# Performance work log

Measured on AMD Instinct MI355X. Metric: run time of the kernel, lower is better.

The kernel has to match this reference:

```python
import jax, jax.numpy as jnp
from jax import lax
import numpy as np

B, TIN, F, H, TOUT = 256, 512, 64, 512, 64


def setup_inputs() -> dict:
    key = jax.random.key(0)
    ks = jax.random.split(key, 16)
    s = 0.05

    def p(k, shape):
        return jax.random.normal(k, shape, jnp.float32) * s

    inp = {
        "x": jax.random.normal(ks[0], (B, TIN, F), jnp.float32),
        "y": jax.random.normal(ks[1], (B, TOUT), jnp.float32),
    }
    i = 2
    for name, insz in [("enc0", F), ("enc1", H), ("dec0", 1), ("dec1", H)]:
        inp[name + "_Wih"] = p(ks[i], (4 * H, insz)); i += 1
        inp[name + "_Whh"] = p(ks[i], (4 * H, H)); i += 1
        inp[name + "_bih"] = jnp.zeros((4 * H,), jnp.float32)
        inp[name + "_bhh"] = jnp.zeros((4 * H,), jnp.float32)
    inp["proj_W"] = p(ks[i], (1, H)); i += 1
    inp["proj_b"] = jnp.zeros((1,), jnp.float32)
    return inp


def _cell(xt, h, c, Wih, Whh, bih, bhh):
    # PyTorch gate order: i, f, g, o
    g = xt @ Wih.T + h @ Whh.T + bih + bhh  # [B, 4H]
    i, f, gg, o = jnp.split(g, 4, axis=-1)
    c = jax.nn.sigmoid(f) * c + jax.nn.sigmoid(i) * jnp.tanh(gg)
    h = jax.nn.sigmoid(o) * jnp.tanh(c)
    return h, c


def reference(x, y,
              enc0_Wih, enc0_Whh, enc0_bih, enc0_bhh,
              enc1_Wih, enc1_Whh, enc1_bih, enc1_bhh,
              dec0_Wih, dec0_Whh, dec0_bih, dec0_bhh,
              dec1_Wih, dec1_Whh, dec1_bih, dec1_bhh,
              proj_W, proj_b):
    Bsz = x.shape[0]
    Hd = enc0_Whh.shape[1]
    Tout = y.shape[1]
    z = jnp.zeros((Bsz, Hd), x.dtype)

    def enc_step(carry, xt):
        h0, c0, h1, c1 = carry
        h0, c0 = _cell(xt, h0, c0, enc0_Wih, enc0_Whh, enc0_bih, enc0_bhh)
        h1, c1 = _cell(h0, h1, c1, enc1_Wih, enc1_Whh, enc1_bih, enc1_bhh)
        return (h0, c0, h1, c1), None

    (h0, c0, h1, c1), _ = lax.scan(enc_step, (z, z, z, z), jnp.swapaxes(x, 0, 1))

    prev = x[:, -1, -1:]  # [B, 1]

    def dec_step(carry, _):
        h0, c0, h1, c1, prev = carry
        h0, c0 = _cell(prev, h0, c0, dec0_Wih, dec0_Whh, dec0_bih, dec0_bhh)
        h1, c1 = _cell(h0, h1, c1, dec1_Wih, dec1_Whh, dec1_bih, dec1_bhh)
        step = h1 @ proj_W.T + proj_b  # [B, 1]
        # teacher_forcing = 0.0 -> always feed model prediction back
        return (h0, c0, h1, c1, step), step[:, 0]

    _, outs = lax.scan(dec_step, (h0, c0, h1, c1, prev), None, length=Tout)
    return outs.T  # [B, Tout]
```

## Files before the change

### kernel.cpp

```cpp
#include <hip/hip_runtime.h>

#define TINN 512
#define FF 64
#define HHD 512
#define TOUTN 64

using v8h = __attribute__((ext_vector_type(8))) _Float16;
using v4h = __attribute__((ext_vector_type(4))) _Float16;
using v4f = __attribute__((ext_vector_type(4))) float;
using u32x4 = __attribute__((ext_vector_type(4))) unsigned int;
using u64 = unsigned long long;

#define AGT __HIP_MEMORY_SCOPE_AGENT

#define WOFF 0
#define BIAS_OFF 131072
#define WIH0_OFF 131328
#define PREV_OFF 131584
#define PART_OFF 131840
#define PROJW_OFF 132864
#define PROJB_OFF 134912
#define TRANS_OFF 134976
#define SMEM_TOTAL 137024

#define WS_BAR 0
#define WS_FLAG_BYTES (4 * 64 * 64 * 64)
#define WS_HOFF WS_FLAG_BYTES
#define HBYTES (256 * HHD * 2)
#define WS_XS (WS_HOFF + 6 * HBYTES)
#define XS_TBYTES 32768
#define WS_NEED (WS_XS + (size_t)TINN * XS_TBYTES)

static __device__ __forceinline__ float sigm(float x) { return 1.0f / (1.0f + __expf(-x)); }
static __device__ __forceinline__ float tanh_f(float x) { return 1.0f - 2.0f / (1.0f + __expf(2.0f * x)); }

static __device__ __forceinline__ v8h aload16(const _Float16* p) {
  union { u64 u[2]; v8h h; } c;
  const u64* q = (const u64*)p;
  c.u[0] = __hip_atomic_load(q, __ATOMIC_RELAXED, AGT);
  c.u[1] = __hip_atomic_load(q + 1, __ATOMIC_RELAXED, AGT);
  return c.h;
}
static __device__ __forceinline__ void astore8(_Float16* p, v4h v) {
  union { u64 u; v4h h; } c;
  c.h = v;
  __hip_atomic_store((u64*)p, c.u, __ATOMIC_RELAXED, AGT);
}
static __device__ __forceinline__ void astore8z(void* p) {
  __hip_atomic_store((u64*)p, 0ull, __ATOMIC_RELAXED, AGT);
}

#if __has_builtin(__builtin_amdgcn_raw_ptr_buffer_load_b128) && \
    __has_builtin(__builtin_amdgcn_make_buffer_rsrc)
#define HAVE_BUFLOAD 1
using rsrc_t = __amdgpu_buffer_rsrc_t;
static __device__ __forceinline__ rsrc_t mkrsrc(const void* p) {
  return __builtin_amdgcn_make_buffer_rsrc((void*)p, (short)0, 0xFFFFFFFFu, 0x00020000);
}
static __device__ __forceinline__ v8h bload16(rsrc_t r, int byteOff) {
  union { u32x4 u; v8h h; } c;
  c.u = __builtin_amdgcn_raw_ptr_buffer_load_b128(r, byteOff, 0, 17);
  return c.h;
}
#endif

static __device__ __forceinline__ void signalDone(unsigned* flagsG, int mySlot, unsigned val) {
  __builtin_amdgcn_s_waitcnt(0);
  __syncthreads();
  if (threadIdx.x < 64) {
    unsigned* p = flagsG + ((size_t)threadIdx.x * 64 + mySlot) * 16;
    __hip_atomic_store(p, val, __ATOMIC_RELAXED, AGT);
  }
}

static __device__ __forceinline__ void waitRolePriv(unsigned* myflags, int base, int tgt) {
  if (tgt > 0) {
    if (threadIdx.x < 32) {
      unsigned* p = myflags + (size_t)(base + threadIdx.x) * 16;
      while ((int)__hip_atomic_load(p, __ATOMIC_RELAXED, AGT) < tgt)
        __builtin_amdgcn_s_sleep(1);
    }
    __syncthreads();
#if __has_builtin(__builtin_amdgcn_sched_barrier)
    __builtin_amdgcn_sched_barrier(0);
#endif
  }
}

static __device__ __forceinline__ void waitRolesPriv(unsigned* myflags, int tgt0, int tgt1) {
  int t = threadIdx.x;
  if (t < 64) {
    int tgt = (t < 32) ? tgt0 : tgt1;
    if (tgt > 0) {
      unsigned* p = myflags + (size_t)t * 16;
      while ((int)__hip_atomic_load(p, __ATOMIC_RELAXED, AGT) < tgt)
        __builtin_amdgcn_s_sleep(1);
    }
  }
  __syncthreads();
#if __has_builtin(__builtin_amdgcn_sched_barrier)
  __builtin_amdgcn_sched_barrier(0);
#endif
}

static __device__ __attribute__((noinline)) void loadWeights(
    int tid, int hc0, const float* W1, int ld1, int K1,
    const float* W2, int K) {
  extern __shared__ char smem[];
  int c = tid >> 2, sub = tid & 3;
  int nt = c >> 4, l = c & 15;
  int n = nt * HHD + hc0 + l;
  int Kq = K >> 2;
  for (int k = sub * Kq; k < (sub + 1) * Kq; ++k) {
    float v;
    if (k < K1) v = W1[(size_t)n * ld1 + k];
    else        v = W2[(size_t)n * HHD + (k - K1)];
    int kc = k >> 6, ks = (k >> 5) & 1, quad = (k >> 3) & 3, j = k & 7;
    int off = (((kc * 2 + ks) * 4 + nt) * 64 + quad * 16 + l) * 16 + j * 2;
    *(_Float16*)(smem + WOFF + off) = (_Float16)v;
  }
}

template <int WC0>
static __device__ __forceinline__ void mfma8(
    const _Float16* src, int rt, int lane, const char* wbLane, v4f* acc) {
#if HAVE_BUFLOAD
  rsrc_t rs = mkrsrc(src);
#endif
#pragma unroll
  for (int kc = 0; kc < 8; ++kc) {
    int off = rt * 16384 + kc * 2048 + lane * 16;
    v8h ak0, ak1;
#if HAVE_BUFLOAD
    ak0 = bload16(rs, off);
    ak1 = bload16(rs, off + 1024);
#else
    ak0 = aload16(src + off / 2);
    ak1 = aload16(src + (off + 1024) / 2);
#endif
    const char* bb = wbLane + (size_t)(WC0 + kc) * 8192;
#pragma unroll
    for (int ks = 0; ks < 2; ++ks) {
      v8h a = ks ? ak1 : ak0;
      acc[0] = __builtin_amdgcn_mfma_f32_16x16x32_f16(a, *(const v8h*)(bb + (ks * 4 + 0) * 1024), acc[0], 0, 0, 0);
      acc[1] = __builtin_amdgcn_mfma_f32_16x16x32_f16(a, *(const v8h*)(bb + (ks * 4 + 1) * 1024), acc[1], 0, 0, 0);
      acc[2] = __builtin_amdgcn_mfma_f32_16x16x32_f16(a, *(const v8h*)(bb + (ks * 4 + 2) * 1024), acc[2], 0, 0, 0);
      acc[3] = __builtin_amdgcn_mfma_f32_16x16x32_f16(a, *(const v8h*)(bb + (ks * 4 + 3) * 1024), acc[3], 0, 0, 0);
    }
  }
}

static __device__ __forceinline__ void mfmaDual(
    const _Float16* h0src, const _Float16* h1src, int rt, int lane,
    const char* wbLane, v4f* acc) {
  v8h a1[16], a0[16];
#if HAVE_BUFLOAD
  rsrc_t r1 = mkrsrc(h1src);
  rsrc_t r0 = mkrsrc(h0src);
#pragma unroll
  for (int kc = 0; kc < 8; ++kc) {
    int off = rt * 16384 + kc * 2048 + lane * 16;
    a1[2 * kc]     = bload16(r1, off);
    a1[2 * kc + 1] = bload16(r1, off + 1024);
  }
#pragma unroll
  for (int kc = 0; kc < 8; ++kc) {
    int off = rt * 16384 + kc * 2048 + lane * 16;
    a0[2 * kc]     = bload16(r0, off);
    a0[2 * kc + 1] = bload16(r0, off + 1024);
  }
#else
#pragma unroll
  for (int kc = 0; kc < 8; ++kc) {
    int off = rt * 16384 + kc * 2048 + lane * 16;
    a1[2 * kc]     = aload16(h1src + off / 2);
    a1[2 * kc + 1] = aload16(h1src + (off + 1024) / 2);
  }
#pragma unroll
  for (int kc = 0; kc < 8; ++kc) {
    int off = rt * 16384 + kc * 2048 + lane * 16;
    a0[2 * kc]     = aload16(h0src + off / 2);
    a0[2 * kc + 1] = aload16(h0src + (off + 1024) / 2);
  }
#endif
#pragma unroll
  for (int kc = 0; kc < 8; ++kc) {
    const char* bb = wbLane + (size_t)(8 + kc) * 8192;
#pragma unroll
    for (int ks = 0; ks < 2; ++ks) {
      v8h a = a1[2 * kc + ks];
      acc[0] = __builtin_amdgcn_mfma_f32_16x16x32_f16(a, *(const v8h*)(bb + (ks * 4 + 0) * 1024), acc[0], 0, 0, 0);
      acc[1] = __builtin_amdgcn_mfma_f32_16x16x32_f16(a, *(const v8h*)(bb + (ks * 4 + 1) * 1024), acc[1], 0, 0, 0);
      acc[2] = __builtin_amdgcn_mfma_f32_16x16x32_f16(a, *(const v8h*)(bb + (ks * 4 + 2) * 1024), acc[2], 0, 0, 0);
      acc[3] = __builtin_amdgcn_mfma_f32_16x16x32_f16(a, *(const v8h*)(bb + (ks * 4 + 3) * 1024), acc[3], 0, 0, 0);
    }
  }
#pragma unroll
  for (int kc = 0; kc < 8; ++kc) {
    const char* bb = wbLane + (size_t)kc * 8192;
#pragma unroll
    for (int ks = 0; ks < 2; ++ks) {
      v8h a = a0[2 * kc + ks];
      acc[0] = __builtin_amdgcn_mfma_f32_16x16x32_f16(a, *(const v8h*)(bb + (ks * 4 + 0) * 1024), acc[0], 0, 0, 0);
      acc[1] = __builtin_amdgcn_mfma_f32_16x16x32_f16(a, *(const v8h*)(bb + (ks * 4 + 1) * 1024), acc[1], 0, 0, 0);
      acc[2] = __builtin_amdgcn_mfma_f32_16x16x32_f16(a, *(const v8h*)(bb + (ks * 4 + 2) * 1024), acc[2], 0, 0, 0);
      acc[3] = __builtin_amdgcn_mfma_f32_16x16x32_f16(a, *(const v8h*)(bb + (ks * 4 + 3) * 1024), acc[3], 0, 0, 0);
    }
  }
}

static __device__ __forceinline__ void xChunk(
    const char* xsT, const float* xstep, int m0, int tid,
    const char* wbLane, v4f* acc) {
  int lane = tid & 63, wave = tid >> 6;
  int l15 = lane & 15, quad = lane >> 4;
  v8h ak0, ak1;
  if (xsT != nullptr) {
    int rt = (m0 >> 4) + wave;
    const char* xb = xsT + rt * 2048 + lane * 16;
    ak0 = *(const v8h*)(xb);
    ak1 = *(const v8h*)(xb + 1024);
  } else {
    int ra = m0 + wave * 16 + l15;
    const float* xr = xstep + (size_t)ra * (TINN * FF) + quad * 8;
    v4f f00 = *(const v4f*)(xr);
    v4f f01 = *(const v4f*)(xr + 4);
    v4f f10 = *(const v4f*)(xr + 32);
    v4f f11 = *(const v4f*)(xr + 36);
#pragma unroll
    for (int e = 0; e < 4; ++e) {
      ak0[e] = (_Float16)f00[e]; ak0[4 + e] = (_Float16)f01[e];
      ak1[e] = (_Float16)f10[e]; ak1[4 + e] = (_Float16)f11[e];
    }
  }
#pragma unroll
  for (int ks = 0; ks < 2; ++ks) {
    v8h a = ks ? ak1 : ak0;
    acc[0] = __builtin_amdgcn_mfma_f32_16x16x32_f16(a, *(const v8h*)(wbLane + (ks * 4 + 0) * 1024), acc[0], 0, 0, 0);
    acc[1] = __builtin_amdgcn_mfma_f32_16x16x32_f16(a, *(const v8h*)(wbLane + (ks * 4 + 1) * 1024), acc[1], 0, 0, 0);
    acc[2] = __builtin_amdgcn_mfma_f32_16x16x32_f16(a, *(const v8h*)(wbLane + (ks * 4 + 2) * 1024), acc[2], 0, 0, 0);
    acc[3] = __builtin_amdgcn_mfma_f32_16x16x32_f16(a, *(const v8h*)(wbLane + (ks * 4 + 3) * 1024), acc[3], 0, 0, 0);
  }
}

static __device__ __forceinline__ void epilogue(
    int tid, int m0, int hc0, int rank1, _Float16* hout, float* creg, v4f* acc) {
  extern __shared__ char smem[];
  int lane = tid & 63, wave = tid >> 6;
  int l15 = lane & 15, quad = lane >> 4;
  float* bias = (float*)(smem + BIAS_OFF);
  float bi = bias[l15], bf = bias[16 + l15], bg = bias[32 + l15], bo = bias[48 + l15];
  float wi = 0.f, wf = 0.f, wg = 0.f, wo = 0.f;
  if (rank1) {
    float* wih0 = (float*)(smem + WIH0_OFF);
    wi = wih0[l15]; wf = wih0[16 + l15]; wg = wih0[32 + l15]; wo = wih0[48 + l15];
  }
  float* prevl = (float*)(smem + PREV_OFF);
  _Float16* tb = (_Float16*)(smem + TRANS_OFF + (size_t)wave * 512);
#pragma unroll
  for (int r = 0; r < 4; ++r) {
    int mloc = wave * 16 + quad * 4 + r;
    float gi = acc[0][r] + bi, gf = acc[1][r] + bf;
    float gg = acc[2][r] + bg, go = acc[3][r] + bo;
    if (rank1) {
      float pv = prevl[mloc];
      gi += pv * wi; gf += pv * wf; gg += pv * wg; go += pv * wo;
    }
    float cc = sigm(gf) * creg[r] + sigm(gi) * tanh_f(gg);
    float h = sigm(go) * tanh_f(cc);
    creg[r] = cc;
    tb[(quad * 4 + r) * 16 + l15] = (_Float16)h;
  }
  {
    int mloc = lane & 15, cg = lane >> 4;
    v4h hv = *(const v4h*)(tb + mloc * 16 + cg * 4);
    int m = m0 + wave * 16 + mloc;
    int c0 = hc0 + cg * 4;
    int off = (m >> 4) * 16384 + (c0 >> 6) * 2048 + ((c0 >> 5) & 1) * 1024 +
              ((c0 >> 3) & 3) * 256 + (m & 15) * 16 + (c0 & 7) * 2;
    astore8((_Float16*)((char*)hout + off), hv);
  }
}


static __device__ __attribute__((noinline)) void stepEnc0(
    int tid, int m0, int hc0, unsigned* flagsG, unsigned* myflags, int mySlot, int p,
    const char* xsT, const float* xstep,
    const _Float16* h0prev, _Float16* h0out, float* creg) {
  extern __shared__ char smem[];
  int lane = tid & 63, wave = tid >> 6;
  v4f acc[4];
  acc[0] = v4f{0.f, 0.f, 0.f, 0.f}; acc[1] = acc[0]; acc[2] = acc[0]; acc[3] = acc[0];
  const char* wbLane = smem + WOFF + (size_t)lane * 16;
  if (p == 0) {
    waitRolesPriv(myflags, 1, 0);
    xChunk(xsT, xstep, m0, tid, wbLane, acc);
  } else {
    xChunk(xsT, xstep, m0, tid, wbLane, acc);
    waitRolesPriv(myflags, p + 1, p - 2);
  }
  mfma8<1>(h0prev, (m0 >> 4) + wave, lane, wbLane, acc);
  epilogue(tid, m0, hc0, 0, h0out, creg, acc);
  signalDone(flagsG, mySlot, p + 2);
}

static __device__ __attribute__((noinline)) void stepL1(
    int tid, int m0, int hc0, unsigned* flagsG, unsigned* myflags, int mySlot,
    int tR1, int tR0,
    const _Float16* h0src, const _Float16* h1prev, _Float16* h1out, float* creg) {
  extern __shared__ char smem[];
  int lane = tid & 63, wave = tid >> 6;
  v4f acc[4];
  acc[0] = v4f{0.f, 0.f, 0.f, 0.f}; acc[1] = acc[0]; acc[2] = acc[0]; acc[3] = acc[0];
  const char* wbLane = smem + WOFF + (size_t)lane * 16;
  int rt = (m0 >> 4) + wave;
  waitRolesPriv(myflags, tR0, tR1);
  mfmaDual(h0src, h1prev, rt, lane, wbLane, acc);
  epilogue(tid, m0, hc0, 0, h1out, creg, acc);
  signalDone(flagsG, mySlot, tR0);
}

static __device__ __attribute__((noinline)) void stepDec0(
    int tid, int m0, int hc0, unsigned* flagsG, unsigned* myflags, int mySlot, int u,
    const _Float16* h0prev, _Float16* h0out, float* creg) {
  extern __shared__ char smem[];
  int lane = tid & 63, wave = tid >> 6;
  v4f acc[4];
  acc[0] = v4f{0.f, 0.f, 0.f, 0.f}; acc[1] = acc[0]; acc[2] = acc[0]; acc[3] = acc[0];
  const char* wbLane = smem + WOFF + (size_t)lane * 16;
  waitRolePriv(myflags, 0, u + 1);
  mfma8<0>(h0prev, (m0 >> 4) + wave, lane, wbLane, acc);
  epilogue(tid, m0, hc0, 1, h0out, creg, acc);
  signalDone(flagsG, mySlot, u + 2);
}

__global__ void __launch_bounds__(256, 1)
seq2seq_kernel(const float* x,
               const float* e0wi, const float* e0wh, const float* e0bi, const float* e0bh,
               const float* e1wi, const float* e1wh, const float* e1bi, const float* e1bh,
               const float* d0wi, const float* d0wh, const float* d0bi, const float* d0bh,
               const float* d1wi, const float* d1wh, const float* d1bi, const float* d1bh,
               const float* pw, const float* pb,
               float* out, char* ws, int useXs) {
  extern __shared__ char smem[];
  int tid = threadIdx.x, bid = blockIdx.x;
  int group = bid >> 6;
  int r = bid & 63;
  bool isL1 = (r >= 32);
  int hcTile = r & 31;
  int hc0 = hcTile * 16;
  int m0 = group * 64;
  unsigned* flagsG = (unsigned*)(ws + WS_BAR) + (size_t)group * 64 * 64 * 16;
  unsigned* myflags = flagsG + (size_t)r * 64 * 16;
  int mySlot = isL1 ? 32 + hcTile : hcTile;
  char* xs = useXs ? (ws + WS_XS) : nullptr;

  _Float16* h0b[4]; _Float16* h1b[2];
  h0b[0] = (_Float16*)(ws + WS_HOFF);
  h0b[1] = (_Float16*)(ws + WS_HOFF + 1 * HBYTES);
  h0b[2] = (_Float16*)(ws + WS_HOFF + 2 * HBYTES);
  h0b[3] = (_Float16*)(ws + WS_HOFF + 3 * HBYTES);
  h1b[0] = (_Float16*)(ws + WS_HOFF + 4 * HBYTES);
  h1b[1] = (_Float16*)(ws + WS_HOFF + 5 * HBYTES);

  float creg[4];
  creg[0] = 0.f; creg[1] = 0.f; creg[2] = 0.f; creg[3] = 0.f;

  {
    int t16 = r * 256 + tid;
    char* base = (t16 < 8192) ? (char*)h0b[3] : (char*)h1b[1];
    int idx = t16 & 8191;
    astore8z(base + (size_t)m0 * HHD * 2 + (size_t)idx * 8);
  }

  if (xs) {
    int m = m0 + (tid & 63);
    int cb = (tid >> 6) * 16;
    int rt = m >> 4, l15m = m & 15;
    for (int k = 0; k < 8; ++k) {
      int t = r + k * 64;
      const float* xp = x + (size_t)m * (TINN * FF) + (size_t)t * FF + cb;
      v4f f0 = *(const v4f*)(xp);
      v4f f1 = *(const v4f*)(xp + 4);
      v4f f2 = *(const v4f*)(xp + 8);
      v4f f3 = *(const v4f*)(xp + 12);
      v4h h0_, h1_, h2_, h3_;
#pragma unroll
      for (int e = 0; e < 4; ++e) {
        h0_[e] = (_Float16)f0[e]; h1_[e] = (_Float16)f1[e];
        h2_[e] = (_Float16)f2[e]; h3_[e] = (_Float16)f3[e];
      }
      char* xt = xs + (size_t)t * XS_TBYTES;
      v4h hs[4] = {h0_, h1_, h2_, h3_};
#pragma unroll
      for (int s = 0; s < 4; ++s) {
        int c0 = cb + 4 * s;
        int off = (rt * 2 + ((c0 >> 5) & 1)) * 1024 +
                  ((c0 >> 3) & 3) * 256 + l15m * 16 + (c0 & 7) * 2;
        astore8((_Float16*)(xt + off), hs[s]);
      }
    }
  }

  if (!isL1) {
    loadWeights(tid, hc0, e0wi, 64, 64, e0wh, 576);
    if (tid < 64) {
      int n = (tid >> 4) * HHD + hc0 + (tid & 15);
      ((float*)(smem + BIAS_OFF))[tid] = e0bi[n] + e0bh[n];
    }
  } else {
    loadWeights(tid, hc0, e1wi, 512, 512, e1wh, 1024);
    if (tid < 64) {
      int n = (tid >> 4) * HHD + hc0 + (tid & 15);
      ((float*)(smem + BIAS_OFF))[tid] = e1bi[n] + e1bh[n];
    }
  }
  signalDone(flagsG, mySlot, 1);

  if (!isL1) {
    for (int p = 0; p < TINN; ++p)
      stepEnc0(tid, m0, hc0, flagsG, myflags, mySlot, p,
               xs ? xs + (size_t)p * XS_TBYTES : nullptr,
               xs ? nullptr : x + (size_t)p * FF,
               h0b[(p + 3) & 3], h0b[p & 3], creg);
    loadWeights(tid, hc0, d0wh, 512, 512, nullptr, 512);
    if (tid < 64) {
      int n = (tid >> 4) * HHD + hc0 + (tid & 15);
      ((float*)(smem + BIAS_OFF))[tid] = d0bi[n] + d0bh[n];
      ((float*)(smem + WIH0_OFF))[tid] = d0wi[n];
    }
    for (int k = tid; k < 512; k += 256) ((float*)(smem + PROJW_OFF))[k] = pw[k];
    if (tid == 0) ((float*)(smem + PROJB_OFF))[0] = pb[0];
    for (int t = 0; t <= TOUTN; ++t) {
      int u = TINN + t;
      waitRolePriv(myflags, 32, u + 1);
      float* prevl = (float*)(smem + PREV_OFF);
      if (t == 0) {
        if (tid < 64)
          prevl[tid] = x[(size_t)(m0 + tid) * (TINN * FF) + 511 * 64 + 63];
      } else {
        float* part = (float*)(smem + PART_OFF);
        float* pjw = (float*)(smem + PROJW_OFF);
        const _Float16* h1base = h1b[(u + 1) & 1];
        int m = m0 + (tid >> 2);
        int rt = m >> 4, l15m = m & 15;
        int kc0 = (tid & 3) * 2;
        float s = 0.f;
#pragma unroll
        for (int kc = kc0; kc < kc0 + 2; ++kc)
#pragma unroll
          for (int ks = 0; ks < 2; ++ks)
#pragma unroll
            for (int q = 0; q < 4; ++q) {
              int off = (rt * 8 + kc) * 2048 + ks * 1024 + q * 256 + l15m * 16;
              v8h hv = aload16(h1base + off / 2);
              const float* w = pjw + kc * 64 + ks * 32 + q * 8;
#pragma unroll
              for (int e = 0; e < 8; ++e) s += (float)hv[e] * w[e];
            }
        part[tid] = s;
        __syncthreads();
        if (tid < 64) {
          float p4 = part[tid * 4] + part[tid * 4 + 1] + part[tid * 4 + 2] +
                     part[tid * 4 + 3] + ((float*)(smem + PROJB_OFF))[0];
          prevl[tid] = p4;
          if (hcTile == 0) out[(size_t)(m0 + tid) * TOUTN + (t - 1)] = p4;
        }
      }
      __syncthreads();
      if (t < TOUTN)
        stepDec0(tid, m0, hc0, flagsG, myflags, mySlot, u,
                 h0b[(u + 3) & 3], h0b[u & 3], creg);
    }
  } else {
    for (int s = 0; s < TINN; ++s)
      stepL1(tid, m0, hc0, flagsG, myflags, mySlot, s + 1, s + 2,
             h0b[s & 3], h1b[(s + 1) & 1], h1b[s & 1], creg);
    loadWeights(tid, hc0, d1wi, 512, 512, d1wh, 1024);
    if (tid < 64) {
      int n = (tid >> 4) * HHD + hc0 + (tid & 15);
      ((float*)(smem + BIAS_OFF))[tid] = d1bi[n] + d1bh[n];
    }
    for (int t = 0; t < TOUTN; ++t) {
      int u = TINN + t;
      stepL1(tid, m0, hc0, flagsG, myflags, mySlot, u + 1, u + 2,
             h0b[u & 3], h1b[(u + 1) & 1], h1b[u & 1], creg);
    }
  }
}

extern "C" void kernel_launch(void* const* d_in, const int* in_sizes, int n_in,
                              void* d_out, int out_size, void* d_ws, size_t ws_size,
                              hipStream_t stream) {
  const float* x = (const float*)d_in[0];
  const float* e0wi = (const float*)d_in[2];
  const float* e0wh = (const float*)d_in[3];
  const float* e0bi = (const float*)d_in[4];
  const float* e0bh = (const float*)d_in[5];
  const float* e1wi = (const float*)d_in[6];
  const float* e1wh = (const float*)d_in[7];
  const float* e1bi = (const float*)d_in[8];
  const float* e1bh = (const float*)d_in[9];
  const float* d0wi = (const float*)d_in[10];
  const float* d0wh = (const float*)d_in[11];
  const float* d0bi = (const float*)d_in[12];
  const float* d0bh = (const float*)d_in[13];
  const float* d1wi = (const float*)d_in[14];
  const float* d1wh = (const float*)d_in[15];
  const float* d1bi = (const float*)d_in[16];
  const float* d1bh = (const float*)d_in[17];
  const float* pw = (const float*)d_in[18];
  const float* pb = (const float*)d_in[19];

  int useXs = (ws_size >= WS_NEED) ? 1 : 0;
  (void)hipFuncSetAttribute((const void*)seq2seq_kernel,
                            hipFuncAttributeMaxDynamicSharedMemorySize, SMEM_TOTAL);
  (void)hipMemsetAsync(d_ws, 0, WS_FLAG_BYTES, stream);
  seq2seq_kernel<<<dim3(256), dim3(256), SMEM_TOTAL, stream>>>(
      x, e0wi, e0wh, e0bi, e0bh, e1wi, e1wh, e1bi, e1bh,
      d0wi, d0wh, d0bi, d0bh, d1wi, d1wh, d1bi, d1bh,
      pw, pb, (float*)d_out, (char*)d_ws, useXs);
}
```

Measured before the change: 4.453 ms.

## Map batch groups onto XCDs and use L2-cached loads for same-XCD exchange

Workgroups are remapped so each batch group's 64 blocks fall on paired XCDs. A startup census reads the hardware XCC_ID to detect which producer roles share the consumer's XCD. Hidden states are written twice, to a local copy read with L2-cached buffer loads and to a remote copy read with coherent loads, and flags use cached polling or plain stores when the role is co-located. The aim is to cut cross-die coherence latency in the per-step recurrent handoff. The precomputed fp16 x transpose is dropped and x is converted inline. Correctness depends on block placement assumptions and on the census handshake, and the dual writes add store traffic.

```diff
diff --git a/kernel.cpp b/kernel.cpp
--- a/kernel.cpp
+++ b/kernel.cpp
@@ -21,18 +21,24 @@
 #define PROJW_OFF 132864
 #define PROJB_OFF 134912
 #define TRANS_OFF 134976
-#define SMEM_TOTAL 137024
-
-#define WS_BAR 0
+#define XCD_OFF 137024
+#define FL_OFF 137280
+#define SMEM_TOTAL 137344
+
 #define WS_FLAG_BYTES (4 * 64 * 64 * 64)
-#define WS_HOFF WS_FLAG_BYTES
+#define WS_CENSUS WS_FLAG_BYTES
+#define WS_CENSUS_BYTES (4 * 64 * 64)
+#define WS_HOFF (WS_FLAG_BYTES + WS_CENSUS_BYTES)
 #define HBYTES (256 * HHD * 2)
-#define WS_XS (WS_HOFF + 6 * HBYTES)
-#define XS_TBYTES 32768
-#define WS_NEED (WS_XS + (size_t)TINN * XS_TBYTES)
 
 static __device__ __forceinline__ float sigm(float x) { return 1.0f / (1.0f + __expf(-x)); }
 static __device__ __forceinline__ float tanh_f(float x) { return 1.0f - 2.0f / (1.0f + __expf(2.0f * x)); }
+
+static __device__ __forceinline__ void schedBar() {
+#if __has_builtin(__builtin_amdgcn_sched_barrier)
+  __builtin_amdgcn_sched_barrier(0);
+#endif
+}
 
 static __device__ __forceinline__ v8h aload16(const _Float16* p) {
   union { u64 u[2]; v8h h; } c;
@@ -57,50 +63,88 @@
 static __device__ __forceinline__ rsrc_t mkrsrc(const void* p) {
   return __builtin_amdgcn_make_buffer_rsrc((void*)p, (short)0, 0xFFFFFFFFu, 0x00020000);
 }
-static __device__ __forceinline__ v8h bload16(rsrc_t r, int byteOff) {
+static __device__ __forceinline__ v8h bload16_b(rsrc_t r, int byteOff) {
   union { u32x4 u; v8h h; } c;
   c.u = __builtin_amdgcn_raw_ptr_buffer_load_b128(r, byteOff, 0, 17);
   return c.h;
 }
-#endif
-
-static __device__ __forceinline__ void signalDone(unsigned* flagsG, int mySlot, unsigned val) {
-  __builtin_amdgcn_s_waitcnt(0);
-  __syncthreads();
-  if (threadIdx.x < 64) {
-    unsigned* p = flagsG + ((size_t)threadIdx.x * 64 + mySlot) * 16;
+static __device__ __forceinline__ v8h bload16_l(rsrc_t r, int byteOff) {
+  union { u32x4 u; v8h h; } c;
+  c.u = __builtin_amdgcn_raw_ptr_buffer_load_b128(r, byteOff, 0, 1);
+  return c.h;
+}
+static __device__ __forceinline__ unsigned flagLoadL2(const unsigned* p) {
+  union { u32x4 u; } c;
+  c.u = __builtin_amdgcn_raw_ptr_buffer_load_b128(mkrsrc(p), 0, 0, 1);
+  return c.u[0];
+}
+#else
+#define HAVE_BUFLOAD 0
+#endif
+
+static __device__ __forceinline__ int getXcc() {
+  int x;
+  asm volatile("s_getreg_b32 %0, hwreg(HW_REG_XCC_ID)" : "=s"(x));
+  return x & 15;
+}
+
+static __device__ __forceinline__ void signalStep(
+    unsigned* flagsG, int mySlot, unsigned val, const char* flagLoc) {
+  asm volatile("s_waitcnt vmcnt(1) lgkmcnt(0)" ::: "memory");
+  schedBar();
+  __builtin_amdgcn_s_barrier();
+  int t = threadIdx.x;
+  bool lane = t < 64;
+  bool fl = lane && (flagLoc[t & 63] != 0);
+  unsigned* p = flagsG + ((size_t)(t & 63) * 64 + mySlot) * 16;
+  if (fl) *p = val;
+  asm volatile("s_waitcnt vmcnt(0) lgkmcnt(0)" ::: "memory");
+  schedBar();
+  __builtin_amdgcn_s_barrier();
+  if (lane && !fl)
     __hip_atomic_store(p, val, __ATOMIC_RELAXED, AGT);
-  }
-}
-
-static __device__ __forceinline__ void waitRolePriv(unsigned* myflags, int base, int tgt) {
-  if (tgt > 0) {
-    if (threadIdx.x < 32) {
-      unsigned* p = myflags + (size_t)(base + threadIdx.x) * 16;
-      while ((int)__hip_atomic_load(p, __ATOMIC_RELAXED, AGT) < tgt)
-        __builtin_amdgcn_s_sleep(1);
-    }
-    __syncthreads();
-#if __has_builtin(__builtin_amdgcn_sched_barrier)
-    __builtin_amdgcn_sched_barrier(0);
-#endif
-  }
-}
-
-static __device__ __forceinline__ void waitRolesPriv(unsigned* myflags, int tgt0, int tgt1) {
+}
+static __device__ __forceinline__ void signalInit(
+    unsigned* flagsG, int mySlot, unsigned val, const char* flagLoc) {
+  asm volatile("s_waitcnt vmcnt(0) lgkmcnt(0)" ::: "memory");
+  schedBar();
+  signalStep(flagsG, mySlot, val, flagLoc);
+}
+
+static __device__ __forceinline__ void pollSlot(unsigned* p, int tgt, bool loc) {
+  for (;;) {
+    unsigned v;
+#if HAVE_BUFLOAD
+    if (loc) v = flagLoadL2(p);
+    else
+#endif
+      v = __hip_atomic_load(p, __ATOMIC_RELAXED, AGT);
+    if ((int)v >= tgt) break;
+    asm volatile("" ::: "memory");
+    __builtin_amdgcn_s_sleep(1);
+  }
+}
+
+static __device__ __forceinline__ void waitRolesPriv(
+    unsigned* myflags, int tgt0, int tgt1, bool loc0, bool loc1) {
   int t = threadIdx.x;
   if (t < 64) {
     int tgt = (t < 32) ? tgt0 : tgt1;
-    if (tgt > 0) {
-      unsigned* p = myflags + (size_t)t * 16;
-      while ((int)__hip_atomic_load(p, __ATOMIC_RELAXED, AGT) < tgt)
-        __builtin_amdgcn_s_sleep(1);
-    }
+    if (tgt > 0)
+      pollSlot(myflags + (size_t)t * 16, tgt, (t < 32) ? loc0 : loc1);
   }
   __syncthreads();
-#if __has_builtin(__builtin_amdgcn_sched_barrier)
-  __builtin_amdgcn_sched_barrier(0);
-#endif
+  schedBar();
+}
+static __device__ __forceinline__ void waitRolePriv(
+    unsigned* myflags, int base, int tgt, bool loc) {
+  if (tgt > 0) {
+    int t = threadIdx.x;
+    if (t < 32)
+      pollSlot(myflags + (size_t)(base + t) * 16, tgt, loc);
+    __syncthreads();
+    schedBar();
+  }
 }
 
 static __device__ __attribute__((noinline)) void loadWeights(
@@ -121,7 +165,7 @@
   }
 }
 
-template <int WC0>
+template <int WC0, bool LOCAL>
 static __device__ __forceinline__ void mfma8(
     const _Float16* src, int rt, int lane, const char* wbLane, v4f* acc) {
 #if HAVE_BUFLOAD
@@ -132,8 +176,8 @@
     int off = rt * 16384 + kc * 2048 + lane * 16;
     v8h ak0, ak1;
 #if HAVE_BUFLOAD
-    ak0 = bload16(rs, off);
-    ak1 = bload16(rs, off + 1024);
+    if constexpr (LOCAL) { ak0 = bload16_l(rs, off); ak1 = bload16_l(rs, off + 1024); }
+    else                 { ak0 = bload16_b(rs, off); ak1 = bload16_b(rs, off + 1024); }
 #else
     ak0 = aload16(src + off / 2);
     ak1 = aload16(src + (off + 1024) / 2);
@@ -150,6 +194,7 @@
   }
 }
 
+template <bool LOC0, bool LOC1>
 static __device__ __forceinline__ void mfmaDual(
     const _Float16* h0src, const _Float16* h1src, int rt, int lane,
     const char* wbLane, v4f* acc) {
@@ -160,14 +205,14 @@
 #pragma unroll
   for (int kc = 0; kc < 8; ++kc) {
     int off = rt * 16384 + kc * 2048 + lane * 16;
-    a1[2 * kc]     = bload16(r1, off);
-    a1[2 * kc + 1] = bload16(r1, off + 1024);
+    if constexpr (LOC1) { a1[2 * kc] = bload16_l(r1, off); a1[2 * kc + 1] = bload16_l(r1, off + 1024); }
+    else                { a1[2 * kc] = bload16_b(r1, off); a1[2 * kc + 1] = bload16_b(r1, off + 1024); }
   }
 #pragma unroll
   for (int kc = 0; kc < 8; ++kc) {
     int off = rt * 16384 + kc * 2048 + lane * 16;
-    a0[2 * kc]     = bload16(r0, off);
-    a0[2 * kc + 1] = bload16(r0, off + 1024);
+    if constexpr (LOC0) { a0[2 * kc] = bload16_l(r0, off); a0[2 * kc + 1] = bload16_l(r0, off + 1024); }
+    else                { a0[2 * kc] = bload16_b(r0, off); a0[2 * kc + 1] = bload16_b(r0, off + 1024); }
   }
 #else
 #pragma unroll
@@ -210,28 +255,20 @@
 }
 
 static __device__ __forceinline__ void xChunk(
-    const char* xsT, const float* xstep, int m0, int tid,
-    const char* wbLane, v4f* acc) {
+    const float* xstep, int m0, int tid, const char* wbLane, v4f* acc) {
   int lane = tid & 63, wave = tid >> 6;
   int l15 = lane & 15, quad = lane >> 4;
   v8h ak0, ak1;
-  if (xsT != nullptr) {
-    int rt = (m0 >> 4) + wave;
-    const char* xb = xsT + rt * 2048 + lane * 16;
-    ak0 = *(const v8h*)(xb);
-    ak1 = *(const v8h*)(xb + 1024);
-  } else {
-    int ra = m0 + wave * 16 + l15;
-    const float* xr = xstep + (size_t)ra * (TINN * FF) + quad * 8;
-    v4f f00 = *(const v4f*)(xr);
-    v4f f01 = *(const v4f*)(xr + 4);
-    v4f f10 = *(const v4f*)(xr + 32);
-    v4f f11 = *(const v4f*)(xr + 36);
-#pragma unroll
-    for (int e = 0; e < 4; ++e) {
-      ak0[e] = (_Float16)f00[e]; ak0[4 + e] = (_Float16)f01[e];
-      ak1[e] = (_Float16)f10[e]; ak1[4 + e] = (_Float16)f11[e];
-    }
+  int ra = m0 + wave * 16 + l15;
+  const float* xr = xstep + (size_t)ra * (TINN * FF) + quad * 8;
+  v4f f00 = *(const v4f*)(xr);
+  v4f f01 = *(const v4f*)(xr + 4);
+  v4f f10 = *(const v4f*)(xr + 32);
+  v4f f11 = *(const v4f*)(xr + 36);
+#pragma unroll
+  for (int e = 0; e < 4; ++e) {
+    ak0[e] = (_Float16)f00[e]; ak0[4 + e] = (_Float16)f01[e];
+    ak1[e] = (_Float16)f10[e]; ak1[4 + e] = (_Float16)f11[e];
   }
 #pragma unroll
   for (int ks = 0; ks < 2; ++ks) {
@@ -244,7 +281,8 @@
 }
 
 static __device__ __forceinline__ void epilogue(
-    int tid, int m0, int hc0, int rank1, _Float16* hout, float* creg, v4f* acc) {
+    int tid, int m0, int hc0, int rank1, _Float16* houtL, _Float16* houtR,
+    float* creg, v4f* acc) {
   extern __shared__ char smem[];
   int lane = tid & 63, wave = tid >> 6;
   int l15 = lane & 15, quad = lane >> 4;
@@ -278,60 +316,70 @@
     int c0 = hc0 + cg * 4;
     int off = (m >> 4) * 16384 + (c0 >> 6) * 2048 + ((c0 >> 5) & 1) * 1024 +
               ((c0 >> 3) & 3) * 256 + (m & 15) * 16 + (c0 & 7) * 2;
-    astore8((_Float16*)((char*)hout + off), hv);
+    *(v4h*)((char*)houtL + off) = hv;
+    schedBar();
+    astore8((_Float16*)((char*)houtR + off), hv);
   }
 }
 
 
 static __device__ __attribute__((noinline)) void stepEnc0(
     int tid, int m0, int hc0, unsigned* flagsG, unsigned* myflags, int mySlot, int p,
-    const char* xsT, const float* xstep,
-    const _Float16* h0prev, _Float16* h0out, float* creg) {
+    const float* xstep, const _Float16* h0prev, _Float16* h0outL, _Float16* h0outR,
+    float* creg, const char* flagLoc, bool loc0, bool loc1) {
   extern __shared__ char smem[];
   int lane = tid & 63, wave = tid >> 6;
   v4f acc[4];
   acc[0] = v4f{0.f, 0.f, 0.f, 0.f}; acc[1] = acc[0]; acc[2] = acc[0]; acc[3] = acc[0];
   const char* wbLane = smem + WOFF + (size_t)lane * 16;
-  if (p == 0) {
-    waitRolesPriv(myflags, 1, 0);
-    xChunk(xsT, xstep, m0, tid, wbLane, acc);
-  } else {
-    xChunk(xsT, xstep, m0, tid, wbLane, acc);
-    waitRolesPriv(myflags, p + 1, p - 2);
-  }
-  mfma8<1>(h0prev, (m0 >> 4) + wave, lane, wbLane, acc);
-  epilogue(tid, m0, hc0, 0, h0out, creg, acc);
-  signalDone(flagsG, mySlot, p + 2);
+  xChunk(xstep, m0, tid, wbLane, acc);
+  waitRolesPriv(myflags, p + 1, p - 2, loc0, loc1);
+  int rt = (m0 >> 4) + wave;
+  if (loc0) mfma8<1, true >(h0prev, rt, lane, wbLane, acc);
+  else      mfma8<1, false>(h0prev, rt, lane, wbLane, acc);
+  epilogue(tid, m0, hc0, 0, h0outL, h0outR, creg, acc);
+  signalStep(flagsG, mySlot, p + 2, flagLoc);
 }
 
 static __device__ __attribute__((noinline)) void stepL1(
     int tid, int m0, int hc0, unsigned* flagsG, unsigned* myflags, int mySlot,
     int tR1, int tR0,
-    const _Float16* h0src, const _Float16* h1prev, _Float16* h1out, float* creg) {
+    const _Float16* h0src, const _Float16* h1prev,
+    _Float16* h1outL, _Float16* h1outR, float* creg,
+    const char* flagLoc, bool loc0, bool loc1) {
   extern __shared__ char smem[];
   int lane = tid & 63, wave = tid >> 6;
   v4f acc[4];
   acc[0] = v4f{0.f, 0.f, 0.f, 0.f}; acc[1] = acc[0]; acc[2] = acc[0]; acc[3] = acc[0];
   const char* wbLane = smem + WOFF + (size_t)lane * 16;
   int rt = (m0 >> 4) + wave;
-  waitRolesPriv(myflags, tR0, tR1);
-  mfmaDual(h0src, h1prev, rt, lane, wbLane, acc);
-  epilogue(tid, m0, hc0, 0, h1out, creg, acc);
-  signalDone(flagsG, mySlot, tR0);
+  waitRolesPriv(myflags, tR0, tR1, loc0, loc1);
+  if (loc0) {
+    if (loc1) mfmaDual<true,  true >(h0src, h1prev, rt, lane, wbLane, acc);
+    else      mfmaDual<true,  false>(h0src, h1prev, rt, lane, wbLane, acc);
+  } else {
+    if (loc1) mfmaDual<false, true >(h0src, h1prev, rt, lane, wbLane, acc);
+    else      mfmaDual<false, false>(h0src, h1prev, rt, lane, wbLane, acc);
+  }
+  epilogue(tid, m0, hc0, 0, h1outL, h1outR, creg, acc);
+  signalStep(flagsG, mySlot, tR0, flagLoc);
 }
 
 static __device__ __attribute__((noinline)) void stepDec0(
     int tid, int m0, int hc0, unsigned* flagsG, unsigned* myflags, int mySlot, int u,
-    const _Float16* h0prev, _Float16* h0out, float* creg) {
+    const _Float16* h0prev, _Float16* h0outL, _Float16* h0outR, float* creg,
+    const char* flagLoc, bool loc0) {
   extern __shared__ char smem[];
   int lane = tid & 63, wave = tid >> 6;
   v4f acc[4];
   acc[0] = v4f{0.f, 0.f, 0.f, 0.f}; acc[1] = acc[0]; acc[2] = acc[0]; acc[3] = acc[0];
   const char* wbLane = smem + WOFF + (size_t)lane * 16;
-  waitRolePriv(myflags, 0, u + 1);
-  mfma8<0>(h0prev, (m0 >> 4) + wave, lane, wbLane, acc);
-  epilogue(tid, m0, hc0, 1, h0out, creg, acc);
-  signalDone(flagsG, mySlot, u + 2);
+  waitRolePriv(myflags, 0, u + 1, loc0);
+  int rt = (m0 >> 4) + wave;
+  if (loc0) mfma8<0, true >(h0prev, rt, lane, wbLane, acc);
+  else      mfma8<0, false>(h0prev, rt, lane, wbLane, acc);
+  epilogue(tid, m0, hc0, 1, h0outL, h0outR, creg, acc);
+  signalStep(flagsG, mySlot, u + 2, flagLoc);
 }
 
 __global__ void __launch_bounds__(256, 1)
@@ -341,66 +389,79 @@
                const float* d0wi, const float* d0wh, const float* d0bi, const float* d0bh,
                const float* d1wi, const float* d1wh, const float* d1bi, const float* d1bh,
                const float* pw, const float* pb,
-               float* out, char* ws, int useXs) {
+               float* out, char* ws) {
   extern __shared__ char smem[];
   int tid = threadIdx.x, bid = blockIdx.x;
-  int group = bid >> 6;
-  int r = bid & 63;
+  int xcd8 = bid & 7, idx = bid >> 3;
+  int group = xcd8 >> 1;
+  int r = (xcd8 & 1) * 32 + idx;
   bool isL1 = (r >= 32);
   int hcTile = r & 31;
   int hc0 = hcTile * 16;
   int m0 = group * 64;
-  unsigned* flagsG = (unsigned*)(ws + WS_BAR) + (size_t)group * 64 * 64 * 16;
+  unsigned* flagsG = (unsigned*)ws + (size_t)group * 64 * 64 * 16;
   unsigned* myflags = flagsG + (size_t)r * 64 * 16;
   int mySlot = isL1 ? 32 + hcTile : hcTile;
-  char* xs = useXs ? (ws + WS_XS) : nullptr;
-
-  _Float16* h0b[4]; _Float16* h1b[2];
-  h0b[0] = (_Float16*)(ws + WS_HOFF);
-  h0b[1] = (_Float16*)(ws + WS_HOFF + 1 * HBYTES);
-  h0b[2] = (_Float16*)(ws + WS_HOFF + 2 * HBYTES);
-  h0b[3] = (_Float16*)(ws + WS_HOFF + 3 * HBYTES);
-  h1b[0] = (_Float16*)(ws + WS_HOFF + 4 * HBYTES);
-  h1b[1] = (_Float16*)(ws + WS_HOFF + 5 * HBYTES);
+
+  char* hb = ws + WS_HOFF;
 
   float creg[4];
   creg[0] = 0.f; creg[1] = 0.f; creg[2] = 0.f; creg[3] = 0.f;
 
   {
     int t16 = r * 256 + tid;
-    char* base = (t16 < 8192) ? (char*)h0b[3] : (char*)h1b[1];
-    int idx = t16 & 8191;
-    astore8z(base + (size_t)m0 * HHD * 2 + (size_t)idx * 8);
-  }
-
-  if (xs) {
-    int m = m0 + (tid & 63);
-    int cb = (tid >> 6) * 16;
-    int rt = m >> 4, l15m = m & 15;
-    for (int k = 0; k < 8; ++k) {
-      int t = r + k * 64;
-      const float* xp = x + (size_t)m * (TINN * FF) + (size_t)t * FF + cb;
-      v4f f0 = *(const v4f*)(xp);
-      v4f f1 = *(const v4f*)(xp + 4);
-      v4f f2 = *(const v4f*)(xp + 8);
-      v4f f3 = *(const v4f*)(xp + 12);
-      v4h h0_, h1_, h2_, h3_;
-#pragma unroll
-      for (int e = 0; e < 4; ++e) {
-        h0_[e] = (_Float16)f0[e]; h1_[e] = (_Float16)f1[e];
-        h2_[e] = (_Float16)f2[e]; h3_[e] = (_Float16)f3[e];
+    int slot = (t16 < 8192) ? 3 : 5;
+    int idx8 = t16 & 8191;
+    size_t o = (size_t)m0 * HHD * 2 + (size_t)idx8 * 8;
+    astore8z(hb + (size_t)slot * HBYTES + o);
+    astore8z(hb + (size_t)(6 + slot) * HBYTES + o);
+  }
+
+  int myXcd = getXcc();
+  {
+    unsigned* census = (unsigned*)(ws + WS_CENSUS) + (size_t)group * 64 * 16;
+    if (tid == 0)
+      __hip_atomic_store(&census[(size_t)r * 16], (unsigned)(myXcd | 256),
+                         __ATOMIC_RELAXED, AGT);
+    int* sX = (int*)(smem + XCD_OFF);
+    if (tid < 64) {
+      unsigned v;
+      unsigned* p = &census[(size_t)tid * 16];
+      for (;;) {
+        v = __hip_atomic_load(p, __ATOMIC_RELAXED, AGT);
+        if (v & 256) break;
+        __builtin_amdgcn_s_sleep(1);
       }
-      char* xt = xs + (size_t)t * XS_TBYTES;
-      v4h hs[4] = {h0_, h1_, h2_, h3_};
-#pragma unroll
-      for (int s = 0; s < 4; ++s) {
-        int c0 = cb + 4 * s;
-        int off = (rt * 2 + ((c0 >> 5) & 1)) * 1024 +
-                  ((c0 >> 3) & 3) * 256 + l15m * 16 + (c0 & 7) * 2;
-        astore8((_Float16*)(xt + off), hs[s]);
-      }
-    }
-  }
+      sX[tid] = (int)(v & 255);
+    }
+    __syncthreads();
+  }
+  const int* sX = (const int*)(smem + XCD_OFF);
+  bool loc0 = true, loc1 = true;
+  for (int i = 0; i < 32; ++i)  loc0 = loc0 && (sX[i] == myXcd);
+  for (int i = 32; i < 64; ++i) loc1 = loc1 && (sX[i] == myXcd);
+  {
+    int cnt = 0;
+    for (int i = 0; i < 64; ++i) cnt += (sX[i] == myXcd) ? 1 : 0;
+    if (cnt > 32) { loc0 = false; loc1 = false; }
+  }
+#if !HAVE_BUFLOAD
+  loc0 = false; loc1 = false;
+#endif
+  {
+    char* fl = (char*)(smem + FL_OFF);
+    if (tid < 64) {
+      int lo = isL1 ? 32 : 0, hi = isL1 ? 64 : 32;
+      bool f = true;
+      for (int j = lo; j < hi; ++j) f = f && (sX[j] == sX[tid]);
+#if !HAVE_BUFLOAD
+      f = false;
+#endif
+      fl[tid] = f ? 1 : 0;
+    }
+    __syncthreads();
+  }
+  const char* flagLoc = (const char*)(smem + FL_OFF);
 
   if (!isL1) {
     loadWeights(tid, hc0, e0wi, 64, 64, e0wh, 576);
@@ -415,14 +476,19 @@
       ((float*)(smem + BIAS_OFF))[tid] = e1bi[n] + e1bh[n];
     }
   }
-  signalDone(flagsG, mySlot, 1);
+  signalInit(flagsG, mySlot, 1, flagLoc);
 
   if (!isL1) {
-    for (int p = 0; p < TINN; ++p)
-      stepEnc0(tid, m0, hc0, flagsG, myflags, mySlot, p,
-               xs ? xs + (size_t)p * XS_TBYTES : nullptr,
-               xs ? nullptr : x + (size_t)p * FF,
-               h0b[(p + 3) & 3], h0b[p & 3], creg);
+    for (int p = 0; p < TINN; ++p) {
+      int sp = (p + 3) & 3, so = p & 3;
+      const _Float16* h0prev =
+          (const _Float16*)(hb + (size_t)(loc0 ? sp : 6 + sp) * HBYTES);
+      stepEnc0(tid, m0, hc0, flagsG, myflags, mySlot, p, x + (size_t)p * FF,
+               h0prev,
+               (_Float16*)(hb + (size_t)so * HBYTES),
+               (_Float16*)(hb + (size_t)(6 + so) * HBYTES),
+               creg, flagLoc, loc0, loc1);
+    }
     loadWeights(tid, hc0, d0wh, 512, 512, nullptr, 512);
     if (tid < 64) {
       int n = (tid >> 4) * HHD + hc0 + (tid & 15);
@@ -431,9 +497,10 @@
     }
     for (int k = tid; k < 512; k += 256) ((float*)(smem + PROJW_OFF))[k] = pw[k];
     if (tid == 0) ((float*)(smem + PROJB_OFF))[0] = pb[0];
+    __syncthreads();
     for (int t = 0; t <= TOUTN; ++t) {
       int u = TINN + t;
-      waitRolePriv(myflags, 32, u + 1);
+      waitRolePriv(myflags, 32, u + 1, loc1);
       float* prevl = (float*)(smem + PREV_OFF);
       if (t == 0) {
         if (tid < 64)
@@ -441,7 +508,8 @@
       } else {
         float* part = (float*)(smem + PART_OFF);
         float* pjw = (float*)(smem + PROJW_OFF);
-        const _Float16* h1base = h1b[(u + 1) & 1];
+        const _Float16* h1base =
+            (const _Float16*)(hb + (size_t)(6 + 4 + ((u + 1) & 1)) * HBYTES);
         int m = m0 + (tid >> 2);
         int rt = m >> 4, l15m = m & 15;
         int kc0 = (tid & 3) * 2;
@@ -468,14 +536,26 @@
         }
       }
       __syncthreads();
-      if (t < TOUTN)
-        stepDec0(tid, m0, hc0, flagsG, myflags, mySlot, u,
-                 h0b[(u + 3) & 3], h0b[u & 3], creg);
+      if (t < TOUTN) {
+        int sp = (u + 3) & 3, so = u & 3;
+        const _Float16* h0prev =
+            (const _Float16*)(hb + (size_t)(loc0 ? sp : 6 + sp) * HBYTES);
+        stepDec0(tid, m0, hc0, flagsG, myflags, mySlot, u, h0prev,
+                 (_Float16*)(hb + (size_t)so * HBYTES),
+                 (_Float16*)(hb + (size_t)(6 + so) * HBYTES),
+                 creg, flagLoc, loc0);
+      }
     }
   } else {
-    for (int s = 0; s < TINN; ++s)
+    for (int s = 0; s < TINN; ++s) {
+      int h0s = s & 3, h1p = 4 + ((s + 1) & 1), h1o = 4 + (s & 1);
       stepL1(tid, m0, hc0, flagsG, myflags, mySlot, s + 1, s + 2,
-             h0b[s & 3], h1b[(s + 1) & 1], h1b[s & 1], creg);
+             (const _Float16*)(hb + (size_t)(loc0 ? h0s : 6 + h0s) * HBYTES),
+             (const _Float16*)(hb + (size_t)(loc1 ? h1p : 6 + h1p) * HBYTES),
+             (_Float16*)(hb + (size_t)h1o * HBYTES),
+             (_Float16*)(hb + (size_t)(6 + h1o) * HBYTES),
+             creg, flagLoc, loc0, loc1);
+    }
     loadWeights(tid, hc0, d1wi, 512, 512, d1wh, 1024);
     if (tid < 64) {
       int n = (tid >> 4) * HHD + hc0 + (tid & 15);
@@ -483,8 +563,13 @@
     }
     for (int t = 0; t < TOUTN; ++t) {
       int u = TINN + t;
+      int h0s = u & 3, h1p = 4 + ((u + 1) & 1), h1o = 4 + (u & 1);
       stepL1(tid, m0, hc0, flagsG, myflags, mySlot, u + 1, u + 2,
-             h0b[u & 3], h1b[(u + 1) & 1], h1b[u & 1], creg);
+             (const _Float16*)(hb + (size_t)(loc0 ? h0s : 6 + h0s) * HBYTES),
+             (const _Float16*)(hb + (size_t)(loc1 ? h1p : 6 + h1p) * HBYTES),
+             (_Float16*)(hb + (size_t)h1o * HBYTES),
+             (_Float16*)(hb + (size_t)(6 + h1o) * HBYTES),
+             creg, flagLoc, loc0, loc1);
     }
   }
 }
@@ -512,12 +597,11 @@
   const float* pw = (const float*)d_in[18];
   const float* pb = (const float*)d_in[19];
 
-  int useXs = (ws_size >= WS_NEED) ? 1 : 0;
   (void)hipFuncSetAttribute((const void*)seq2seq_kernel,
                             hipFuncAttributeMaxDynamicSharedMemorySize, SMEM_TOTAL);
-  (void)hipMemsetAsync(d_ws, 0, WS_FLAG_BYTES, stream);
+  (void)hipMemsetAsync(d_ws, 0, WS_FLAG_BYTES + WS_CENSUS_BYTES, stream);
   seq2seq_kernel<<<dim3(256), dim3(256), SMEM_TOTAL, stream>>>(
       x, e0wi, e0wh, e0bi, e0bh, e1wi, e1wh, e1bi, e1bh,
       d0wi, d0wh, d0bi, d0bh, d1wi, d1wh, d1bi, d1bh,
-      pw, pb, (float*)d_out, (char*)d_ws, useXs);
-}
+      pw, pb, (float*)d_out, (char*)d_ws);
+}
```

Measured after the change: 4.572 ms. 2.7% more time.
